# Performance work log

Hardware: AMD Instinct MI355X
Metric: run time of the kernel (lower is better)

## Reference

```python
import jax, jax.numpy as jnp
import numpy as np

N_NODES = 100000
N_EDGES = 1600000
IN_FEATS = 128
H_FEATS = 64
NUM_CLASSES = 40
NEG_SLOPE = 0.2  # DGL GATConv default


def gat_layer(x, src, dst, W, attn_l, attn_r, bias, n_nodes):
    # x: [N, din]; W: [din, dout]; attn_l/r, bias: [dout]
    feat = x @ W                                   # [N, dout]
    el = feat @ attn_l                             # [N]
    er = feat @ attn_r                             # [N]
    e = jax.nn.leaky_relu(el[src] + er[dst], NEG_SLOPE)  # [E]
    # segment softmax over destination nodes (numerically stable)
    m = jax.ops.segment_max(e, dst, num_segments=n_nodes)   # [N]
    ee = jnp.exp(e - m[dst])                                 # [E]
    s = jax.ops.segment_sum(ee, dst, num_segments=n_nodes)  # [N]
    alpha = ee / s[dst]                                      # [E]
    out = jax.ops.segment_sum(alpha[:, None] * feat[src], dst,
                              num_segments=n_nodes)          # [N, dout]
    return out + bias


def setup_inputs() -> dict:
    key = jax.random.key(0)
    ks = jax.random.split(key, 12)
    in_feat = jax.random.normal(ks[0], (N_NODES, IN_FEATS), dtype=jnp.float32)
    src = jax.random.randint(ks[1], (N_EDGES,), 0, N_NODES, dtype=jnp.int32)
    dst = jax.random.randint(ks[2], (N_EDGES,), 0, N_NODES, dtype=jnp.int32)
    def glorot(k, shape):
        fan = sum(shape)
        return jax.random.normal(k, shape, dtype=jnp.float32) * jnp.sqrt(2.0 / fan)
    W1 = glorot(ks[3], (IN_FEATS, H_FEATS))
    al1 = glorot(ks[4], (H_FEATS,)) 
    ar1 = glorot(ks[5], (H_FEATS,))
    b1 = jnp.zeros((H_FEATS,), jnp.float32)
    W2 = glorot(ks[6], (H_FEATS, NUM_CLASSES))
    al2 = glorot(ks[7], (NUM_CLASSES,))
    ar2 = glorot(ks[8], (NUM_CLASSES,))
    b2 = jnp.zeros((NUM_CLASSES,), jnp.float32)
    return {"in_feat": in_feat, "src": src, "dst": dst,
            "W1": W1, "al1": al1, "ar1": ar1, "b1": b1,
            "W2": W2, "al2": al2, "ar2": ar2, "b2": b2}


def reference(in_feat, src, dst, W1, al1, ar1, b1, W2, al2, ar2, b2):
    h = gat_layer(in_feat, src, dst, W1, al1, ar1, b1, N_NODES)  # gat1
    h = jax.nn.elu(h)                                            # F.elu
    h = gat_layer(h, src, dst, W2, al2, ar2, b2, N_NODES)        # gat2
    return h  # [N, num_classes]
```

## Files before the change

kernel.cpp:

```cpp
#include <hip/hip_runtime.h>

#define N_NODES 100000
#define N_EDGES 1600000
#define DB_SHIFT 9
#define DB_SIZE 512
#define NDB 196
#define DB_CAP 10240
#define PART_EDGES 2048
#define NPART ((N_EDGES + PART_EDGES - 1) / PART_EDGES)
#define NGEMM1 ((N_NODES + 63) / 64)

constexpr float NEG_SLOPE = 0.2f;

__device__ __forceinline__ float leaky(float x) { return x > 0.f ? x : NEG_SLOPE * x; }

__device__ __forceinline__ float bflo(unsigned u) { return __uint_as_float(u << 16); }
__device__ __forceinline__ float bfhi(unsigned u) { return __uint_as_float(u & 0xffff0000u); }

__device__ __forceinline__ void bfsplit(float x, short& h, short& l) {
    unsigned u = __float_as_uint(x);
    h = (short)(u >> 16);
    float res = x - __uint_as_float(u & 0xffff0000u);
    unsigned r = __float_as_uint(res);
    r = (r + 0x7fffu + ((r >> 16) & 1u)) >> 16;
    l = (short)r;
}

__global__ void wconv2_kernel(const float* __restrict__ W1, const float* __restrict__ W2,
                              unsigned short* __restrict__ W1Th, unsigned short* __restrict__ W1Tl,
                              unsigned short* __restrict__ W2Th, unsigned short* __restrict__ W2Tl,
                              int* __restrict__ db_cursor) {
    int idx = blockIdx.x * 256 + threadIdx.x;
    if (blockIdx.x == 0 && threadIdx.x < NDB) db_cursor[threadIdx.x] = 0;
    if (idx < 64 * 128) {
        int n = idx / 128, k = idx % 128;
        short h, l;
        bfsplit(W1[(size_t)k * 64 + n], h, l);
        W1Th[idx] = (unsigned short)h;
        W1Tl[idx] = (unsigned short)l;
    } else if (idx < 64 * 128 + 48 * 64) {
        int j = idx - 64 * 128;
        int n = j / 64, k = j % 64;
        float x = (n < 40) ? W2[(size_t)k * 40 + n] : 0.f;
        short h, l;
        bfsplit(x, h, l);
        W2Th[j] = (unsigned short)h;
        W2Tl[j] = (unsigned short)l;
    }
}

template <int DIN, int NOUT, int NTILES, int OSTR>
__device__ __forceinline__ void gemm_mfma_body(
        int bid, const float* __restrict__ X,
        const unsigned short* __restrict__ WTh, const unsigned short* __restrict__ WTl,
        const float* __restrict__ al, const float* __restrict__ ar,
        unsigned short* __restrict__ featb, float* __restrict__ el,
        float* __restrict__ er, int N) {
    constexpr int KT = DIN / 32;
    using frag = __attribute__((ext_vector_type(8))) short;
    using accv = __attribute__((ext_vector_type(4))) float;

    int lane = threadIdx.x & 63;
    int wid = threadIdx.x >> 6;
    int r0 = (bid * 4 + wid) * 16;
    if (r0 >= N) return;
    int m = lane & 15;
    int quad = lane >> 4;
    int row = r0 + m;
    bool rok = row < N;
    const float* xrow = X + (size_t)(rok ? row : 0) * DIN;

    frag ah[KT], alo[KT];
#pragma unroll
    for (int kt = 0; kt < KT; ++kt) {
        float xv[8];
        if (rok) {
            float4 a0 = *reinterpret_cast<const float4*>(xrow + kt * 32 + quad * 8);
            float4 a1 = *reinterpret_cast<const float4*>(xrow + kt * 32 + quad * 8 + 4);
            xv[0] = a0.x; xv[1] = a0.y; xv[2] = a0.z; xv[3] = a0.w;
            xv[4] = a1.x; xv[5] = a1.y; xv[6] = a1.z; xv[7] = a1.w;
        } else {
#pragma unroll
            for (int j = 0; j < 8; ++j) xv[j] = 0.f;
        }
#pragma unroll
        for (int j = 0; j < 8; ++j) {
            short h, l;
            bfsplit(xv[j], h, l);
            ah[kt][j] = h;
            alo[kt][j] = l;
        }
    }

    accv acc[NTILES];
#pragma unroll
    for (int nt = 0; nt < NTILES; ++nt) acc[nt] = (accv){0.f, 0.f, 0.f, 0.f};

#pragma unroll
    for (int nt = 0; nt < NTILES; ++nt) {
        const unsigned short* bh_base = WTh + (size_t)(nt * 16 + m) * DIN;
        const unsigned short* bl_base = WTl + (size_t)(nt * 16 + m) * DIN;
#pragma unroll
        for (int kt = 0; kt < KT; ++kt) {
            frag bh = *reinterpret_cast<const frag*>(bh_base + kt * 32 + quad * 8);
            frag bl = *reinterpret_cast<const frag*>(bl_base + kt * 32 + quad * 8);
            acc[nt] = __builtin_amdgcn_mfma_f32_16x16x32_bf16(ah[kt], bh, acc[nt], 0, 0, 0);
            acc[nt] = __builtin_amdgcn_mfma_f32_16x16x32_bf16(ah[kt], bl, acc[nt], 0, 0, 0);
            acc[nt] = __builtin_amdgcn_mfma_f32_16x16x32_bf16(alo[kt], bh, acc[nt], 0, 0, 0);
        }
    }

    float pel[4] = {0.f, 0.f, 0.f, 0.f};
    float per[4] = {0.f, 0.f, 0.f, 0.f};
#pragma unroll
    for (int nt = 0; nt < NTILES; ++nt) {
        int n = nt * 16 + m;
        float av = (n < NOUT) ? al[n] : 0.f;
        float rv = (n < NOUT) ? ar[n] : 0.f;
#pragma unroll
        for (int reg = 0; reg < 4; ++reg) {
            float v = acc[nt][reg];
            pel[reg] += v * av;
            per[reg] += v * rv;
            int grow = r0 + quad * 4 + reg;
            if (grow < N && n < NOUT) {
                unsigned u = __float_as_uint(v);
                u = (u + 0x7fffu + ((u >> 16) & 1u)) >> 16;
                featb[(size_t)grow * OSTR + n] = (unsigned short)u;
            }
        }
    }
#pragma unroll
    for (int o = 1; o < 16; o <<= 1) {
#pragma unroll
        for (int reg = 0; reg < 4; ++reg) {
            pel[reg] += __shfl_xor(pel[reg], o, 64);
            per[reg] += __shfl_xor(per[reg], o, 64);
        }
    }
    if (m == 0) {
#pragma unroll
        for (int reg = 0; reg < 4; ++reg) {
            int grow = r0 + quad * 4 + reg;
            if (grow < N) { el[grow] = pel[reg]; er[grow] = per[reg]; }
        }
    }
}

__global__ __launch_bounds__(256) void fusedA_kernel(
        const int* __restrict__ src, const int* __restrict__ dst,
        int* __restrict__ db_cursor, unsigned* __restrict__ staged, int E,
        const float* __restrict__ X,
        const unsigned short* __restrict__ W1Th, const unsigned short* __restrict__ W1Tl,
        const float* __restrict__ al, const float* __restrict__ ar,
        unsigned short* __restrict__ featb, float* __restrict__ el,
        float* __restrict__ er, int N) {
    int p = blockIdx.x / 3;
    int r = blockIdx.x % 3;
    if (r == 2) {
        __shared__ unsigned pay_s[PART_EDGES];
        __shared__ unsigned stage[PART_EDGES];
        __shared__ unsigned char bktA[PART_EDGES];
        __shared__ unsigned char bkt_s[PART_EDGES];
        __shared__ unsigned hist[256];
        __shared__ unsigned scanb[256];
        __shared__ unsigned baseg[256];
        __shared__ unsigned cnt[256];
        int tid = threadIdx.x;
        int e0 = p * PART_EDGES;
        hist[tid] = 0;
        cnt[tid] = 0;
        __syncthreads();
#pragma unroll
        for (int k = 0; k < PART_EDGES / 256; ++k) {
            int idx = k * 256 + tid;
            int i = e0 + idx;
            if (i < E) {
                int d = dst[i];
                unsigned b = (unsigned)d >> DB_SHIFT;
                pay_s[idx] = (((unsigned)d & (DB_SIZE - 1)) << 17) | (unsigned)src[i];
                bktA[idx] = (unsigned char)b;
                atomicAdd(&hist[b], 1u);
            }
        }
        __syncthreads();
        unsigned v = hist[tid];
        scanb[tid] = v;
        __syncthreads();
        for (int off = 1; off < 256; off <<= 1) {
            unsigned t = (tid >= off) ? scanb[tid - off] : 0;
            __syncthreads();
            scanb[tid] += t;
            __syncthreads();
        }
        unsigned excl = scanb[tid] - v;
        __syncthreads();
        scanb[tid] = excl;
        if (tid < NDB)
            baseg[tid] = (unsigned)(tid * DB_CAP) + (unsigned)atomicAdd(&db_cursor[tid], (int)v);
        __syncthreads();
#pragma unroll
        for (int k = 0; k < PART_EDGES / 256; ++k) {
            int idx = k * 256 + tid;
            int i = e0 + idx;
            if (i < E) {
                unsigned b = bktA[idx];
                unsigned slot = scanb[b] + atomicAdd(&cnt[b], 1u);
                stage[slot] = pay_s[idx];
                bkt_s[slot] = (unsigned char)b;
            }
        }
        __syncthreads();
        int total = min(PART_EDGES, E - e0);
        for (int j = tid; j < total; j += 256) {
            unsigned b = bkt_s[j];
            unsigned addr = baseg[b] + ((unsigned)j - scanb[b]);
            staged[addr] = stage[j];
        }
    } else {
        gemm_mfma_body<128, 64, 4, 64>(2 * p + r, X, W1Th, W1Tl, al, ar, featb, el, er, N);
    }
}

__global__ __launch_bounds__(256) void bucket_sort_kernel(
        const unsigned* __restrict__ staged, const int* __restrict__ db_cursor,
        int* __restrict__ csr_src, int* __restrict__ row_ptr, int N, int E) {
    __shared__ unsigned pay[DB_CAP];
    __shared__ int sorted[DB_CAP];
    __shared__ int hist[DB_SIZE];
    __shared__ int excl[DB_SIZE];
    __shared__ int psum[256];
    __shared__ int scn[256];
    int tid = threadIdx.x;
    int k = blockIdx.x;
    int c = (tid < NDB) ? db_cursor[tid] : 0;
    scn[tid] = c;
    __syncthreads();
    for (int off = 1; off < 256; off <<= 1) {
        int t = (tid >= off) ? scn[tid - off] : 0;
        __syncthreads();
        scn[tid] += t;
        __syncthreads();
    }
    int cnt = db_cursor[k];
    int base = scn[k] - cnt;
    if (k == 0 && tid == 0) row_ptr[N] = E;

    for (int i = tid; i < DB_SIZE; i += 256) hist[i] = 0;
    __syncthreads();
    for (int j = tid; j < cnt; j += 256) {
        unsigned p = staged[(size_t)k * DB_CAP + j];
        pay[j] = p;
        atomicAdd(&hist[p >> 17], 1);
    }
    __syncthreads();
    int s = hist[2 * tid] + hist[2 * tid + 1];
    psum[tid] = s;
    __syncthreads();
    for (int off = 1; off < 256; off <<= 1) {
        int t = (tid >= off) ? psum[tid - off] : 0;
        __syncthreads();
        psum[tid] += t;
        __syncthreads();
    }
    int e0 = psum[tid] - s;
    excl[2 * tid] = e0;
    excl[2 * tid + 1] = e0 + hist[2 * tid];
    __syncthreads();
    for (int i = tid; i < DB_SIZE; i += 256) {
        int d = k * DB_SIZE + i;
        if (d < N) row_ptr[d] = base + excl[i];
    }
    for (int i = tid; i < DB_SIZE; i += 256) hist[i] = 0;
    __syncthreads();
    for (int j = tid; j < cnt; j += 256) {
        unsigned p = pay[j];
        int dl = (int)(p >> 17);
        int pos = excl[dl] + atomicAdd(&hist[dl], 1);
        sorted[pos] = (int)(p & 0x1FFFFu);
    }
    __syncthreads();
    for (int j = tid; j < cnt; j += 256) csr_src[base + j] = sorted[j];
}

__global__ __launch_bounds__(256) void gemm2_kernel(
        const float* __restrict__ X,
        const unsigned short* __restrict__ WTh, const unsigned short* __restrict__ WTl,
        const float* __restrict__ al, const float* __restrict__ ar,
        unsigned short* __restrict__ featb, float* __restrict__ el,
        float* __restrict__ er, int N) {
    gemm_mfma_body<64, 40, 3, 48>(blockIdx.x, X, WTh, WTl, al, ar, featb, el, er, N);
}

template <int NIT, int G2, int FSTR>
__device__ __forceinline__ void gather_batch(int g, int cl, int s, float ee,
                                             const unsigned short* __restrict__ featb,
                                             float4& acc) {
    float w[NIT];
    int sj[NIT];
#pragma unroll
    for (int i = 0; i < NIT; ++i) {
        int e = 4 * i + g;
        w[i] = __shfl(ee, e, 64);
        sj[i] = __shfl(s, e, 64);
    }
    uint2 q[NIT];
#pragma unroll
    for (int i = 0; i < NIT; ++i) {
        q[i] = make_uint2(0u, 0u);
        if (cl < G2)
            q[i] = *(reinterpret_cast<const uint2*>(featb + (size_t)sj[i] * FSTR) + cl);
    }
#pragma unroll
    for (int i = 0; i < NIT; ++i) {
        acc.x += w[i] * bflo(q[i].x);
        acc.y += w[i] * bfhi(q[i].x);
        acc.z += w[i] * bflo(q[i].y);
        acc.w += w[i] * bfhi(q[i].y);
    }
}

template <int DOUT, int FSTR, int OSTR, bool ELU>
__global__ void agg_kernel(const int* __restrict__ row_ptr, const int* __restrict__ csr_src,
                           const float* __restrict__ el, const float* __restrict__ er,
                           const unsigned short* __restrict__ featb,
                           const float* __restrict__ bias, float* __restrict__ outp, int N) {
    int lane = threadIdx.x & 63;
    int n = blockIdx.x * (blockDim.x >> 6) + (threadIdx.x >> 6);
    if (n >= N) return;
    int beg = row_ptr[n];
    int end = row_ptr[n + 1];
    int deg = end - beg;
    float ern = er[n];

    constexpr int G2 = DOUT / 4;

    if (deg <= 64) {
        int s = 0;
        float e = -1e30f;
        bool act = lane < deg;
        if (act) {
            s = csr_src[beg + lane];
            e = leaky(el[s] + ern);
        }
        float m = e;
#pragma unroll
        for (int o = 32; o > 0; o >>= 1) m = fmaxf(m, __shfl_xor(m, o, 64));
        float ee = act ? __expf(e - m) : 0.f;
        float ssum = ee;
#pragma unroll
        for (int o = 32; o > 0; o >>= 1) ssum += __shfl_xor(ssum, o, 64);

        int g = lane >> 4;
        int cl = lane & 15;
        float4 acc = make_float4(0.f, 0.f, 0.f, 0.f);
        if (deg <= 16) {
            gather_batch<4, G2, FSTR>(g, cl, s, ee, featb, acc);
        } else if (deg <= 32) {
            gather_batch<8, G2, FSTR>(g, cl, s, ee, featb, acc);
        } else {
            int niter = (deg + 3) >> 2;
            for (int i = 0; i < niter; i += 2) {
                int e0 = 4 * i + g;
                int e1 = e0 + 4;
                float w0 = __shfl(ee, e0 & 63, 64);
                int s0 = __shfl(s, e0 & 63, 64);
                float w1 = __shfl(ee, e1 & 63, 64);
                int s1 = __shfl(s, e1 & 63, 64);
                if (e1 >= 64) w1 = 0.f;
                if (cl < G2) {
                    uint2 q0 = *(reinterpret_cast<const uint2*>(featb + (size_t)s0 * FSTR) + cl);
                    uint2 q1 = *(reinterpret_cast<const uint2*>(featb + (size_t)s1 * FSTR) + cl);
                    acc.x += w0 * bflo(q0.x) + w1 * bflo(q1.x);
                    acc.y += w0 * bfhi(q0.x) + w1 * bfhi(q1.x);
                    acc.z += w0 * bflo(q0.y) + w1 * bflo(q1.y);
                    acc.w += w0 * bfhi(q0.y) + w1 * bfhi(q1.y);
                }
            }
        }
#pragma unroll
        for (int o = 16; o <= 32; o <<= 1) {
            acc.x += __shfl_xor(acc.x, o, 64);
            acc.y += __shfl_xor(acc.y, o, 64);
            acc.z += __shfl_xor(acc.z, o, 64);
            acc.w += __shfl_xor(acc.w, o, 64);
        }
        if (g == 0 && cl < G2) {
            float inv = (deg > 0) ? 1.f / ssum : 0.f;
            const float4 b4 = reinterpret_cast<const float4*>(bias)[cl];
            float4 o4;
            o4.x = acc.x * inv + b4.x;
            o4.y = acc.y * inv + b4.y;
            o4.z = acc.z * inv + b4.z;
            o4.w = acc.w * inv + b4.w;
            if (ELU) {
                o4.x = o4.x > 0.f ? o4.x : (__expf(o4.x) - 1.f);
                o4.y = o4.y > 0.f ? o4.y : (__expf(o4.y) - 1.f);
                o4.z = o4.z > 0.f ? o4.z : (__expf(o4.z) - 1.f);
                o4.w = o4.w > 0.f ? o4.w : (__expf(o4.w) - 1.f);
            }
            *reinterpret_cast<float4*>(outp + (size_t)n * OSTR + 4 * cl) = o4;
        }
        return;
    }

    float m = -1e30f;
    for (int j = beg + lane; j < end; j += 64) {
        float e = leaky(el[csr_src[j]] + ern);
        m = fmaxf(m, e);
    }
#pragma unroll
    for (int o = 32; o > 0; o >>= 1) m = fmaxf(m, __shfl_xor(m, o, 64));

    float ssum = 0.f;
    float acc = 0.f;
    for (int base = beg; base < end; base += 64) {
        int j = base + lane;
        int cnt = min(64, end - base);
        int s = (lane < cnt) ? csr_src[j] : 0;
        float ee = 0.f;
        if (lane < cnt) {
            float e = leaky(el[s] + ern);
            ee = __expf(e - m);
        }
        ssum += ee;
        for (int t = 0; t < cnt; ++t) {
            float w = __shfl(ee, t, 64);
            int sj = __shfl(s, t, 64);
            if (lane < DOUT)
                acc += w * __uint_as_float(((unsigned)featb[(size_t)sj * FSTR + lane]) << 16);
        }
    }
#pragma unroll
    for (int o = 32; o > 0; o >>= 1) ssum += __shfl_xor(ssum, o, 64);

    if (lane < DOUT) {
        float o = acc / ssum + bias[lane];
        if (ELU) o = (o > 0.f) ? o : (__expf(o) - 1.f);
        outp[(size_t)n * OSTR + lane] = o;
    }
}

extern "C" void kernel_launch(void* const* d_in, const int* in_sizes, int n_in,
                              void* d_out, int out_size, void* d_ws, size_t ws_size,
                              hipStream_t stream) {
    const float* in_feat = (const float*)d_in[0];
    const int* src = (const int*)d_in[1];
    const int* dst = (const int*)d_in[2];
    const float* W1 = (const float*)d_in[3];
    const float* al1 = (const float*)d_in[4];
    const float* ar1 = (const float*)d_in[5];
    const float* b1 = (const float*)d_in[6];
    const float* W2 = (const float*)d_in[7];
    const float* al2 = (const float*)d_in[8];
    const float* ar2 = (const float*)d_in[9];
    const float* b2 = (const float*)d_in[10];
    float* out = (float*)d_out;

    const int N = N_NODES, E = N_EDGES;

    size_t off = 0;
    auto carve = [&](size_t bytes) {
        void* p = (char*)d_ws + off;
        off += (bytes + 255) & ~(size_t)255;
        return p;
    };
    unsigned short* featb = (unsigned short*)carve((size_t)N * 64 * 2);
    float* el    = (float*)carve((size_t)N * 4);
    float* er    = (float*)carve((size_t)N * 4);
    int* row_ptr = (int*)carve((size_t)(N + 1) * 4);
    int* csr_src = (int*)carve((size_t)E * 4);
    int* db_cursor = (int*)carve((size_t)NDB * 4);
    unsigned short* W1Th = (unsigned short*)carve((size_t)64 * 128 * 2);
    unsigned short* W1Tl = (unsigned short*)carve((size_t)64 * 128 * 2);
    unsigned short* W2Th = (unsigned short*)carve((size_t)48 * 64 * 2);
    unsigned short* W2Tl = (unsigned short*)carve((size_t)48 * 64 * 2);
    size_t offH = off;
    float* h = (float*)carve((size_t)N * 64 * 4);
    size_t off_end = off;
    off = offH;
    unsigned* staged = (unsigned*)carve((size_t)NDB * DB_CAP * 4);
    off = off_end;

    wconv2_kernel<<<(64 * 128 + 48 * 64 + 255) / 256, 256, 0, stream>>>(
        W1, W2, W1Th, W1Tl, W2Th, W2Tl, db_cursor);

    fusedA_kernel<<<3 * NPART, 256, 0, stream>>>(
        src, dst, db_cursor, staged, E,
        in_feat, W1Th, W1Tl, al1, ar1, featb, el, er, N);

    bucket_sort_kernel<<<NDB, 256, 0, stream>>>(staged, db_cursor, csr_src, row_ptr, N, E);

    int agrid = (N + 3) / 4;

    agg_kernel<64, 64, 64, true><<<agrid, 256, 0, stream>>>(row_ptr, csr_src, el, er, featb, b1, h, N);

    gemm2_kernel<<<(N + 63) / 64, 256, 0, stream>>>(h, W2Th, W2Tl, al2, ar2, featb, el, er, N);

    agg_kernel<40, 48, 40, false><<<agrid, 256, 0, stream>>>(row_ptr, csr_src, el, er, featb, b2, out, N);
}
```

Baseline: 269.9 us.

## Stage GEMM rows in LDS, pre-swizzle weights, widen bucket sort and gather

Weights are stored pre-permuted in MFMA fragment order so each lane reads a contiguous 16-byte fragment. X rows for the GEMMs are first loaded into padded shared memory with coalesced float4 loads. The bucket sort kernel moves from 256 to 1024 threads per block. Layer-1 aggregation uses 8 lanes per row with 16-byte loads and more edges in flight. This mixes several independent changes and adds shared-memory pressure and extra barriers.

```diff
diff --git a/kernel.cpp b/kernel.cpp
--- a/kernel.cpp
+++ b/kernel.cpp
@@ -33,56 +33,68 @@
     int idx = blockIdx.x * 256 + threadIdx.x;
     if (blockIdx.x == 0 && threadIdx.x < NDB) db_cursor[threadIdx.x] = 0;
     if (idx < 64 * 128) {
-        int n = idx / 128, k = idx % 128;
+        int n = idx >> 7, k = idx & 127;
+        int nt = n >> 4, m = n & 15;
+        int kt = k >> 5, quad = (k >> 3) & 3, j = k & 7;
+        int off = (((nt * 4 + kt) * 4 + quad) * 16 + m) * 8 + j;
         short h, l;
         bfsplit(W1[(size_t)k * 64 + n], h, l);
-        W1Th[idx] = (unsigned short)h;
-        W1Tl[idx] = (unsigned short)l;
+        W1Th[off] = (unsigned short)h;
+        W1Tl[off] = (unsigned short)l;
     } else if (idx < 64 * 128 + 48 * 64) {
-        int j = idx - 64 * 128;
-        int n = j / 64, k = j % 64;
+        int t = idx - 64 * 128;
+        int n = t >> 6, k = t & 63;
+        int nt = n >> 4, m = n & 15;
+        int kt = k >> 5, quad = (k >> 3) & 3, j = k & 7;
+        int off = (((nt * 2 + kt) * 4 + quad) * 16 + m) * 8 + j;
         float x = (n < 40) ? W2[(size_t)k * 40 + n] : 0.f;
         short h, l;
         bfsplit(x, h, l);
-        W2Th[j] = (unsigned short)h;
-        W2Tl[j] = (unsigned short)l;
-    }
-}
-
-template <int DIN, int NOUT, int NTILES, int OSTR>
+        W2Th[off] = (unsigned short)h;
+        W2Tl[off] = (unsigned short)l;
+    }
+}
+
+template <int DIN, int NOUT, int NTILES, int OSTR, int XSTR>
 __device__ __forceinline__ void gemm_mfma_body(
         int bid, const float* __restrict__ X,
         const unsigned short* __restrict__ WTh, const unsigned short* __restrict__ WTl,
         const float* __restrict__ al, const float* __restrict__ ar,
         unsigned short* __restrict__ featb, float* __restrict__ el,
-        float* __restrict__ er, int N) {
+        float* __restrict__ er, int N, float* XS) {
     constexpr int KT = DIN / 32;
+    constexpr int F4 = DIN / 4;
     using frag = __attribute__((ext_vector_type(8))) short;
     using accv = __attribute__((ext_vector_type(4))) float;
 
-    int lane = threadIdx.x & 63;
-    int wid = threadIdx.x >> 6;
-    int r0 = (bid * 4 + wid) * 16;
+    int tid = threadIdx.x;
+    int rblk = bid * 64;
+
+#pragma unroll
+    for (int it = 0; it < 64 * F4 / 256; ++it) {
+        int idx = it * 256 + tid;
+        int row = idx / F4, c4 = idx % F4;
+        float4 v = make_float4(0.f, 0.f, 0.f, 0.f);
+        if (rblk + row < N)
+            v = reinterpret_cast<const float4*>(X + (size_t)(rblk + row) * DIN)[c4];
+        *reinterpret_cast<float4*>(&XS[row * XSTR + c4 * 4]) = v;
+    }
+    __syncthreads();
+
+    int lane = tid & 63;
+    int wid = tid >> 6;
+    int r0 = rblk + wid * 16;
     if (r0 >= N) return;
     int m = lane & 15;
     int quad = lane >> 4;
-    int row = r0 + m;
-    bool rok = row < N;
-    const float* xrow = X + (size_t)(rok ? row : 0) * DIN;
+    int rowl = wid * 16 + m;
 
     frag ah[KT], alo[KT];
 #pragma unroll
     for (int kt = 0; kt < KT; ++kt) {
-        float xv[8];
-        if (rok) {
-            float4 a0 = *reinterpret_cast<const float4*>(xrow + kt * 32 + quad * 8);
-            float4 a1 = *reinterpret_cast<const float4*>(xrow + kt * 32 + quad * 8 + 4);
-            xv[0] = a0.x; xv[1] = a0.y; xv[2] = a0.z; xv[3] = a0.w;
-            xv[4] = a1.x; xv[5] = a1.y; xv[6] = a1.z; xv[7] = a1.w;
-        } else {
-#pragma unroll
-            for (int j = 0; j < 8; ++j) xv[j] = 0.f;
-        }
+        float4 a0 = *reinterpret_cast<const float4*>(&XS[rowl * XSTR + kt * 32 + quad * 8]);
+        float4 a1 = *reinterpret_cast<const float4*>(&XS[rowl * XSTR + kt * 32 + quad * 8 + 4]);
+        float xv[8] = {a0.x, a0.y, a0.z, a0.w, a1.x, a1.y, a1.z, a1.w};
 #pragma unroll
         for (int j = 0; j < 8; ++j) {
             short h, l;
@@ -98,12 +110,11 @@
 
 #pragma unroll
     for (int nt = 0; nt < NTILES; ++nt) {
-        const unsigned short* bh_base = WTh + (size_t)(nt * 16 + m) * DIN;
-        const unsigned short* bl_base = WTl + (size_t)(nt * 16 + m) * DIN;
 #pragma unroll
         for (int kt = 0; kt < KT; ++kt) {
-            frag bh = *reinterpret_cast<const frag*>(bh_base + kt * 32 + quad * 8);
-            frag bl = *reinterpret_cast<const frag*>(bl_base + kt * 32 + quad * 8);
+            int foff = (((nt * KT + kt) * 4 + quad) * 16 + m) * 8;
+            frag bh = *reinterpret_cast<const frag*>(WTh + foff);
+            frag bl = *reinterpret_cast<const frag*>(WTl + foff);
             acc[nt] = __builtin_amdgcn_mfma_f32_16x16x32_bf16(ah[kt], bh, acc[nt], 0, 0, 0);
             acc[nt] = __builtin_amdgcn_mfma_f32_16x16x32_bf16(ah[kt], bl, acc[nt], 0, 0, 0);
             acc[nt] = __builtin_amdgcn_mfma_f32_16x16x32_bf16(alo[kt], bh, acc[nt], 0, 0, 0);
@@ -155,17 +166,18 @@
         const float* __restrict__ al, const float* __restrict__ ar,
         unsigned short* __restrict__ featb, float* __restrict__ el,
         float* __restrict__ er, int N) {
+    extern __shared__ char smem[];
     int p = blockIdx.x / 3;
     int r = blockIdx.x % 3;
     if (r == 2) {
-        __shared__ unsigned pay_s[PART_EDGES];
-        __shared__ unsigned stage[PART_EDGES];
-        __shared__ unsigned char bktA[PART_EDGES];
-        __shared__ unsigned char bkt_s[PART_EDGES];
-        __shared__ unsigned hist[256];
-        __shared__ unsigned scanb[256];
-        __shared__ unsigned baseg[256];
-        __shared__ unsigned cnt[256];
+        unsigned* pay_s = (unsigned*)smem;
+        unsigned* stage = pay_s + PART_EDGES;
+        unsigned* hist  = stage + PART_EDGES;
+        unsigned* scanb = hist + 256;
+        unsigned* baseg = scanb + 256;
+        unsigned* cnt   = baseg + 256;
+        unsigned char* bktA  = (unsigned char*)(cnt + 256);
+        unsigned char* bkt_s = bktA + PART_EDGES;
         int tid = threadIdx.x;
         int e0 = p * PART_EDGES;
         hist[tid] = 0;
@@ -218,11 +230,14 @@
             staged[addr] = stage[j];
         }
     } else {
-        gemm_mfma_body<128, 64, 4, 64>(2 * p + r, X, W1Th, W1Tl, al, ar, featb, el, er, N);
-    }
-}
-
-__global__ __launch_bounds__(256) void bucket_sort_kernel(
+        int bid = 2 * p + r;
+        if (bid < NGEMM1)
+            gemm_mfma_body<128, 64, 4, 64, 132>(bid, X, W1Th, W1Tl, al, ar, featb, el, er, N,
+                                                (float*)smem);
+    }
+}
+
+__global__ __launch_bounds__(1024) void bucket_sort_kernel(
         const unsigned* __restrict__ staged, const int* __restrict__ db_cursor,
         int* __restrict__ csr_src, int* __restrict__ row_ptr, int N, int E) {
     __shared__ unsigned pay[DB_CAP];
@@ -233,54 +248,55 @@
     __shared__ int scn[256];
     int tid = threadIdx.x;
     int k = blockIdx.x;
-    int c = (tid < NDB) ? db_cursor[tid] : 0;
-    scn[tid] = c;
+    if (tid < 256) scn[tid] = (tid < NDB) ? db_cursor[tid] : 0;
     __syncthreads();
     for (int off = 1; off < 256; off <<= 1) {
-        int t = (tid >= off) ? scn[tid - off] : 0;
-        __syncthreads();
-        scn[tid] += t;
+        int t = (tid < 256 && tid >= off) ? scn[tid - off] : 0;
+        __syncthreads();
+        if (tid < 256) scn[tid] += t;
         __syncthreads();
     }
     int cnt = db_cursor[k];
     int base = scn[k] - cnt;
     if (k == 0 && tid == 0) row_ptr[N] = E;
 
-    for (int i = tid; i < DB_SIZE; i += 256) hist[i] = 0;
-    __syncthreads();
-    for (int j = tid; j < cnt; j += 256) {
+    for (int i = tid; i < DB_SIZE; i += 1024) hist[i] = 0;
+    __syncthreads();
+    for (int j = tid; j < cnt; j += 1024) {
         unsigned p = staged[(size_t)k * DB_CAP + j];
         pay[j] = p;
         atomicAdd(&hist[p >> 17], 1);
     }
     __syncthreads();
-    int s = hist[2 * tid] + hist[2 * tid + 1];
-    psum[tid] = s;
+    int s = 0;
+    if (tid < 256) { s = hist[2 * tid] + hist[2 * tid + 1]; psum[tid] = s; }
     __syncthreads();
     for (int off = 1; off < 256; off <<= 1) {
-        int t = (tid >= off) ? psum[tid - off] : 0;
-        __syncthreads();
-        psum[tid] += t;
-        __syncthreads();
-    }
-    int e0 = psum[tid] - s;
-    excl[2 * tid] = e0;
-    excl[2 * tid + 1] = e0 + hist[2 * tid];
-    __syncthreads();
-    for (int i = tid; i < DB_SIZE; i += 256) {
+        int t = (tid < 256 && tid >= off) ? psum[tid - off] : 0;
+        __syncthreads();
+        if (tid < 256) psum[tid] += t;
+        __syncthreads();
+    }
+    if (tid < 256) {
+        int e0 = psum[tid] - s;
+        excl[2 * tid] = e0;
+        excl[2 * tid + 1] = e0 + hist[2 * tid];
+    }
+    __syncthreads();
+    for (int i = tid; i < DB_SIZE; i += 1024) {
         int d = k * DB_SIZE + i;
         if (d < N) row_ptr[d] = base + excl[i];
     }
-    for (int i = tid; i < DB_SIZE; i += 256) hist[i] = 0;
-    __syncthreads();
-    for (int j = tid; j < cnt; j += 256) {
+    for (int i = tid; i < DB_SIZE; i += 1024) hist[i] = 0;
+    __syncthreads();
+    for (int j = tid; j < cnt; j += 1024) {
         unsigned p = pay[j];
         int dl = (int)(p >> 17);
         int pos = excl[dl] + atomicAdd(&hist[dl], 1);
         sorted[pos] = (int)(p & 0x1FFFFu);
     }
     __syncthreads();
-    for (int j = tid; j < cnt; j += 256) csr_src[base + j] = sorted[j];
+    for (int j = tid; j < cnt; j += 1024) csr_src[base + j] = sorted[j];
 }
 
 __global__ __launch_bounds__(256) void gemm2_kernel(
@@ -289,7 +305,37 @@
         const float* __restrict__ al, const float* __restrict__ ar,
         unsigned short* __restrict__ featb, float* __restrict__ el,
         float* __restrict__ er, int N) {
-    gemm_mfma_body<64, 40, 3, 48>(blockIdx.x, X, WTh, WTl, al, ar, featb, el, er, N);
+    __shared__ float XS2[64 * 68];
+    gemm_mfma_body<64, 40, 3, 48, 68>(blockIdx.x, X, WTh, WTl, al, ar, featb, el, er, N, XS2);
+}
+
+template <int NIT>
+__device__ __forceinline__ void gather8(int g, int cl, int s, float ee,
+                                        const unsigned short* __restrict__ featb,
+                                        float4& accA, float4& accB) {
+    float w[NIT];
+    int sj[NIT];
+#pragma unroll
+    for (int i = 0; i < NIT; ++i) {
+        int e = 8 * i + g;
+        w[i] = __shfl(ee, e, 64);
+        sj[i] = __shfl(s, e, 64);
+    }
+    uint4 q[NIT];
+#pragma unroll
+    for (int i = 0; i < NIT; ++i)
+        q[i] = *reinterpret_cast<const uint4*>(featb + (size_t)sj[i] * 64 + cl * 8);
+#pragma unroll
+    for (int i = 0; i < NIT; ++i) {
+        accA.x += w[i] * bflo(q[i].x);
+        accA.y += w[i] * bfhi(q[i].x);
+        accA.z += w[i] * bflo(q[i].y);
+        accA.w += w[i] * bfhi(q[i].y);
+        accB.x += w[i] * bflo(q[i].z);
+        accB.y += w[i] * bfhi(q[i].z);
+        accB.z += w[i] * bflo(q[i].w);
+        accB.w += w[i] * bfhi(q[i].w);
+    }
 }
 
 template <int NIT, int G2, int FSTR>
@@ -333,8 +379,6 @@
     int deg = end - beg;
     float ern = er[n];
 
-    constexpr int G2 = DOUT / 4;
-
     if (deg <= 64) {
         int s = 0;
         float e = -1e30f;
@@ -351,55 +395,79 @@
 #pragma unroll
         for (int o = 32; o > 0; o >>= 1) ssum += __shfl_xor(ssum, o, 64);
 
-        int g = lane >> 4;
-        int cl = lane & 15;
-        float4 acc = make_float4(0.f, 0.f, 0.f, 0.f);
-        if (deg <= 16) {
-            gather_batch<4, G2, FSTR>(g, cl, s, ee, featb, acc);
-        } else if (deg <= 32) {
-            gather_batch<8, G2, FSTR>(g, cl, s, ee, featb, acc);
+        if constexpr (DOUT == 64) {
+            int g = lane >> 3;
+            int cl = lane & 7;
+            float4 accA = make_float4(0.f, 0.f, 0.f, 0.f);
+            float4 accB = make_float4(0.f, 0.f, 0.f, 0.f);
+            if (deg <= 16) gather8<2>(g, cl, s, ee, featb, accA, accB);
+            else if (deg <= 32) gather8<4>(g, cl, s, ee, featb, accA, accB);
+            else gather8<8>(g, cl, s, ee, featb, accA, accB);
+#pragma unroll
+            for (int o = 8; o <= 32; o <<= 1) {
+                accA.x += __shfl_xor(accA.x, o, 64);
+                accA.y += __shfl_xor(accA.y, o, 64);
+                accA.z += __shfl_xor(accA.z, o, 64);
+                accA.w += __shfl_xor(accA.w, o, 64);
+                accB.x += __shfl_xor(accB.x, o, 64);
+                accB.y += __shfl_xor(accB.y, o, 64);
+                accB.z += __shfl_xor(accB.z, o, 64);
+                accB.w += __shfl_xor(accB.w, o, 64);
+            }
+            if (lane < 8) {
+                float inv = (deg > 0) ? 1.f / ssum : 0.f;
+                const float4 b4a = reinterpret_cast<const float4*>(bias)[2 * cl];
+                const float4 b4b = reinterpret_cast<const float4*>(bias)[2 * cl + 1];
+                float4 oa, ob;
+                oa.x = accA.x * inv + b4a.x; oa.y = accA.y * inv + b4a.y;
+                oa.z = accA.z * inv + b4a.z; oa.w = accA.w * inv + b4a.w;
+                ob.x = accB.x * inv + b4b.x; ob.y = accB.y * inv + b4b.y;
+                ob.z = accB.z * inv + b4b.z; ob.w = accB.w * inv + b4b.w;
+                if (ELU) {
+                    oa.x = oa.x > 0.f ? oa.x : (__expf(oa.x) - 1.f);
+                    oa.y = oa.y > 0.f ? oa.y : (__expf(oa.y) - 1.f);
+                    oa.z = oa.z > 0.f ? oa.z : (__expf(oa.z) - 1.f);
+                    oa.w = oa.w > 0.f ? oa.w : (__expf(oa.w) - 1.f);
+                    ob.x = ob.x > 0.f ? ob.x : (__expf(ob.x) - 1.f);
+                    ob.y = ob.y > 0.f ? ob.y : (__expf(ob.y) - 1.f);
+                    ob.z = ob.z > 0.f ? ob.z : (__expf(ob.z) - 1.f);
+                    ob.w = ob.w > 0.f ? ob.w : (__expf(ob.w) - 1.f);
+                }
+                float* op = outp + (size_t)n * OSTR + cl * 8;
+                *reinterpret_cast<float4*>(op) = oa;
+                *reinterpret_cast<float4*>(op + 4) = ob;
+            }
         } else {
-            int niter = (deg + 3) >> 2;
-            for (int i = 0; i < niter; i += 2) {
-                int e0 = 4 * i + g;
-                int e1 = e0 + 4;
-                float w0 = __shfl(ee, e0 & 63, 64);
-                int s0 = __shfl(s, e0 & 63, 64);
-                float w1 = __shfl(ee, e1 & 63, 64);
-                int s1 = __shfl(s, e1 & 63, 64);
-                if (e1 >= 64) w1 = 0.f;
-                if (cl < G2) {
-                    uint2 q0 = *(reinterpret_cast<const uint2*>(featb + (size_t)s0 * FSTR) + cl);
-                    uint2 q1 = *(reinterpret_cast<const uint2*>(featb + (size_t)s1 * FSTR) + cl);
-                    acc.x += w0 * bflo(q0.x) + w1 * bflo(q1.x);
-                    acc.y += w0 * bfhi(q0.x) + w1 * bfhi(q1.x);
-                    acc.z += w0 * bflo(q0.y) + w1 * bflo(q1.y);
-                    acc.w += w0 * bfhi(q0.y) + w1 * bfhi(q1.y);
+            constexpr int G2 = DOUT / 4;
+            int g = lane >> 4;
+            int cl = lane & 15;
+            float4 acc = make_float4(0.f, 0.f, 0.f, 0.f);
+            if (deg <= 16) gather_batch<4, G2, FSTR>(g, cl, s, ee, featb, acc);
+            else if (deg <= 32) gather_batch<8, G2, FSTR>(g, cl, s, ee, featb, acc);
+            else gather_batch<16, G2, FSTR>(g, cl, s, ee, featb, acc);
+#pragma unroll
+            for (int o = 16; o <= 32; o <<= 1) {
+                acc.x += __shfl_xor(acc.x, o, 64);
+                acc.y += __shfl_xor(acc.y, o, 64);
+                acc.z += __shfl_xor(acc.z, o, 64);
+                acc.w += __shfl_xor(acc.w, o, 64);
+            }
+            if (g == 0 && cl < G2) {
+                float inv = (deg > 0) ? 1.f / ssum : 0.f;
+                const float4 b4 = reinterpret_cast<const float4*>(bias)[cl];
+                float4 o4;
+                o4.x = acc.x * inv + b4.x;
+                o4.y = acc.y * inv + b4.y;
+                o4.z = acc.z * inv + b4.z;
+                o4.w = acc.w * inv + b4.w;
+                if (ELU) {
+                    o4.x = o4.x > 0.f ? o4.x : (__expf(o4.x) - 1.f);
+                    o4.y = o4.y > 0.f ? o4.y : (__expf(o4.y) - 1.f);
+                    o4.z = o4.z > 0.f ? o4.z : (__expf(o4.z) - 1.f);
+                    o4.w = o4.w > 0.f ? o4.w : (__expf(o4.w) - 1.f);
                 }
-            }
-        }
-#pragma unroll
-        for (int o = 16; o <= 32; o <<= 1) {
-            acc.x += __shfl_xor(acc.x, o, 64);
-            acc.y += __shfl_xor(acc.y, o, 64);
-            acc.z += __shfl_xor(acc.z, o, 64);
-            acc.w += __shfl_xor(acc.w, o, 64);
-        }
-        if (g == 0 && cl < G2) {
-            float inv = (deg > 0) ? 1.f / ssum : 0.f;
-            const float4 b4 = reinterpret_cast<const float4*>(bias)[cl];
-            float4 o4;
-            o4.x = acc.x * inv + b4.x;
-            o4.y = acc.y * inv + b4.y;
-            o4.z = acc.z * inv + b4.z;
-            o4.w = acc.w * inv + b4.w;
-            if (ELU) {
-                o4.x = o4.x > 0.f ? o4.x : (__expf(o4.x) - 1.f);
-                o4.y = o4.y > 0.f ? o4.y : (__expf(o4.y) - 1.f);
-                o4.z = o4.z > 0.f ? o4.z : (__expf(o4.z) - 1.f);
-                o4.w = o4.w > 0.f ? o4.w : (__expf(o4.w) - 1.f);
-            }
-            *reinterpret_cast<float4*>(outp + (size_t)n * OSTR + 4 * cl) = o4;
+                *reinterpret_cast<float4*>(outp + (size_t)n * OSTR + 4 * cl) = o4;
+            }
         }
         return;
     }
@@ -485,11 +553,11 @@
     wconv2_kernel<<<(64 * 128 + 48 * 64 + 255) / 256, 256, 0, stream>>>(
         W1, W2, W1Th, W1Tl, W2Th, W2Tl, db_cursor);
 
-    fusedA_kernel<<<3 * NPART, 256, 0, stream>>>(
+    fusedA_kernel<<<3 * NPART, 256, 64 * 132 * 4, stream>>>(
         src, dst, db_cursor, staged, E,
         in_feat, W1Th, W1Tl, al1, ar1, featb, el, er, N);
 
-    bucket_sort_kernel<<<NDB, 256, 0, stream>>>(staged, db_cursor, csr_src, row_ptr, N, E);
+    bucket_sort_kernel<<<NDB, 1024, 0, stream>>>(staged, db_cursor, csr_src, row_ptr, N, E);
 
     int agrid = (N + 3) / 4;
 
```

New measurement: 279.1 us. 1.03x slower.
